# Kernel optimization log

Measured on AMD Instinct MI355X. Metric: run time of the kernel, lower is better.

## Reference

```python
import jax, jax.numpy as jnp
import numpy as np

DIM_QK = 1024


def setup_inputs() -> dict:
    key = jax.random.key(0)
    ks = jax.random.split(key, 5)
    B, S, D = 4, 2048, 1024
    return {
        "x": jax.random.normal(ks[0], (B, S, D), dtype=jnp.float32),
        "Wq": jax.random.normal(ks[1], (DIM_QK, D), dtype=jnp.float32) * (D ** -0.5),
        "Wk": jax.random.normal(ks[2], (DIM_QK, D), dtype=jnp.float32) * (D ** -0.5),
        "Wv": jax.random.normal(ks[3], (D, D), dtype=jnp.float32) * (D ** -0.5),
        "Wo": jax.random.normal(ks[4], (D, D), dtype=jnp.float32) * (D ** -0.5),
    }


def reference(x, Wq, Wk, Wv, Wo):
    # torch Linear: y = x @ W.T (no bias)
    q = jnp.einsum('bsd,kd->bsk', x, Wq)
    k = jnp.einsum('bsd,kd->bsk', x, Wk)
    v = jnp.einsum('bsd,vd->bsv', x, Wv)
    scale = (DIM_QK // 2) ** (-0.5)
    dist = jnp.einsum('bqk,btk->bqt', q, k) * scale  # [B,S,S]
    weight = jax.lax.stop_gradient(dist)             # pre-softmax scores (detached)
    attn = jax.nn.softmax(dist, axis=-1)
    ctx = jnp.einsum('bqt,btv->bqv', attn, v)
    out = jnp.einsum('bqv,ev->bqe', ctx, Wo)
    return (out, weight)
```

## Files before the change

### kernel.cpp

```cpp
#include <hip/hip_runtime.h>
#include <stdint.h>

typedef __attribute__((ext_vector_type(8))) short bf16x8;
typedef __attribute__((ext_vector_type(4))) float f32x4;

__device__ __forceinline__ unsigned short f32_to_bf16(float f) {
  union { float f; unsigned int u; } v; v.f = f;
  unsigned int u = v.u;
  u += 0x7fffu + ((u >> 16) & 1u);
  return (unsigned short)(u >> 16);
}

__device__ __forceinline__ void gload_lds16(const unsigned short* g, unsigned short* lds) {
  __builtin_amdgcn_global_load_lds(
      (const __attribute__((address_space(1))) unsigned int*)g,
      (__attribute__((address_space(3))) unsigned int*)lds,
      16, 0, 0);
}

template<int MODE>
__global__ __launch_bounds__(256, 2)
void gemm_bt(const unsigned short* __restrict__ A,
             const unsigned short* __restrict__ Bm,
             void* __restrict__ Cv,
             int M, int N, int K,
             long sA_, long sB_, long sC_,
             float scale)
{
  __shared__ unsigned short sA[128 * 32];
  __shared__ unsigned short sB[128 * 32];

  const int bz = blockIdx.z;
  const unsigned short* Ab = A + (long)bz * sA_;
  const unsigned short* Bb = Bm + (long)bz * sB_;

  const int m0 = blockIdx.x * 128;
  const int n0 = blockIdx.y * 128;

  const int t = threadIdx.x;
  const int lane = t & 63;
  const int w = t >> 6;
  const int wr = (w >> 1) * 64;
  const int wc = (w & 1) * 64;

  f32x4 acc[4][4];
#pragma unroll
  for (int i = 0; i < 4; ++i)
#pragma unroll
    for (int j = 0; j < 4; ++j)
      acc[i][j] = (f32x4){0.f, 0.f, 0.f, 0.f};

  const int r0 = t >> 2;
  const int kc = (t & 3) * 8;
  const unsigned short* Ap0 = Ab + (long)(m0 + r0) * K + kc;
  const unsigned short* Ap1 = Ab + (long)(m0 + r0 + 64) * K + kc;
  const unsigned short* Bp0 = Bb + (long)(n0 + r0) * K + kc;
  const unsigned short* Bp1 = Bb + (long)(n0 + r0 + 64) * K + kc;

  const int lrow = lane & 15;
  const int q8 = (lane >> 4) * 8;

  for (int k0 = 0; k0 < K; k0 += 32) {
    __syncthreads();
    gload_lds16(Ap0 + k0, &sA[t * 8]);
    gload_lds16(Ap1 + k0, &sA[t * 8 + 2048]);
    gload_lds16(Bp0 + k0, &sB[t * 8]);
    gload_lds16(Bp1 + k0, &sB[t * 8 + 2048]);
    __syncthreads();

    bf16x8 af[4], bfr[4];
#pragma unroll
    for (int i = 0; i < 4; ++i) {
      af[i]  = *(const bf16x8*)&sA[(wr + i * 16 + lrow) * 32 + q8];
      bfr[i] = *(const bf16x8*)&sB[(wc + i * 16 + lrow) * 32 + q8];
    }
#pragma unroll
    for (int mi = 0; mi < 4; ++mi)
#pragma unroll
      for (int ni = 0; ni < 4; ++ni)
        acc[mi][ni] = __builtin_amdgcn_mfma_f32_16x16x32_bf16(af[mi], bfr[ni], acc[mi][ni], 0, 0, 0);
  }

  const int cl = lane & 15;
  const int rq = (lane >> 4) * 4;

  if (MODE == 2) {
    float* Cb = (float*)Cv + (long)bz * sC_;
#pragma unroll
    for (int mi = 0; mi < 4; ++mi) {
      const int rowb = m0 + wr + mi * 16 + rq;
#pragma unroll
      for (int ni = 0; ni < 4; ++ni) {
        const int col = n0 + wc + ni * 16 + cl;
#pragma unroll
        for (int r = 0; r < 4; ++r)
          Cb[(long)(rowb + r) * N + col] = acc[mi][ni][r] * scale;
      }
    }
  } else {
    unsigned short* Cb = (unsigned short*)Cv + (long)bz * sC_;
#pragma unroll
    for (int mi = 0; mi < 4; ++mi) {
      const int rowb = m0 + wr + mi * 16 + rq;
#pragma unroll
      for (int ni = 0; ni < 4; ++ni) {
        const int col = n0 + wc + ni * 16 + cl;
#pragma unroll
        for (int r = 0; r < 4; ++r)
          Cb[(long)(rowb + r) * N + col] = f32_to_bf16(acc[mi][ni][r]);
      }
    }
  }
}

__global__ __launch_bounds__(256)
void softmax_rows(const float* __restrict__ dist, unsigned short* __restrict__ attn) {
  const long row = blockIdx.x;
  const float4* in = (const float4*)(dist + row * 2048);
  const int t = threadIdx.x;
  float4 v0 = in[t];
  float4 v1 = in[t + 256];

  float m = fmaxf(fmaxf(fmaxf(v0.x, v0.y), fmaxf(v0.z, v0.w)),
                  fmaxf(fmaxf(v1.x, v1.y), fmaxf(v1.z, v1.w)));
#pragma unroll
  for (int off = 32; off > 0; off >>= 1)
    m = fmaxf(m, __shfl_xor(m, off, 64));

  __shared__ float redm[4];
  __shared__ float reds[4];
  if ((t & 63) == 0) redm[t >> 6] = m;
  __syncthreads();
  m = fmaxf(fmaxf(redm[0], redm[1]), fmaxf(redm[2], redm[3]));

  float e[8];
  e[0] = __expf(v0.x - m); e[1] = __expf(v0.y - m);
  e[2] = __expf(v0.z - m); e[3] = __expf(v0.w - m);
  e[4] = __expf(v1.x - m); e[5] = __expf(v1.y - m);
  e[6] = __expf(v1.z - m); e[7] = __expf(v1.w - m);

  float s = ((e[0] + e[1]) + (e[2] + e[3])) + ((e[4] + e[5]) + (e[6] + e[7]));
#pragma unroll
  for (int off = 32; off > 0; off >>= 1)
    s += __shfl_xor(s, off, 64);
  if ((t & 63) == 0) reds[t >> 6] = s;
  __syncthreads();
  s = (reds[0] + reds[1]) + (reds[2] + reds[3]);

  const float inv = 1.0f / s;
  ushort4 o0, o1;
  o0.x = f32_to_bf16(e[0] * inv); o0.y = f32_to_bf16(e[1] * inv);
  o0.z = f32_to_bf16(e[2] * inv); o0.w = f32_to_bf16(e[3] * inv);
  o1.x = f32_to_bf16(e[4] * inv); o1.y = f32_to_bf16(e[5] * inv);
  o1.z = f32_to_bf16(e[6] * inv); o1.w = f32_to_bf16(e[7] * inv);
  *(ushort4*)(attn + row * 2048 + t * 4) = o0;
  *(ushort4*)(attn + row * 2048 + 1024 + t * 4) = o1;
}

__global__ __launch_bounds__(256)
void cast_f32_bf16(const float* __restrict__ in, unsigned short* __restrict__ out, int n) {
  const int i = (blockIdx.x * 256 + threadIdx.x) * 4;
  if (i < n) {
    float4 v = *(const float4*)(in + i);
    ushort4 o;
    o.x = f32_to_bf16(v.x); o.y = f32_to_bf16(v.y);
    o.z = f32_to_bf16(v.z); o.w = f32_to_bf16(v.w);
    *(ushort4*)(out + i) = o;
  }
}

extern "C" void kernel_launch(void* const* d_in, const int* in_sizes, int n_in,
                              void* d_out, int out_size, void* d_ws, size_t ws_size,
                              hipStream_t stream) {
  const float* x  = (const float*)d_in[0];
  const float* Wq = (const float*)d_in[1];
  const float* Wk = (const float*)d_in[2];
  const float* Wv = (const float*)d_in[3];
  const float* Wo = (const float*)d_in[4];

  const long Bn = 4, S = 2048, D = 1024;
  const long MS = Bn * S;

  float* out_p  = (float*)d_out;
  float* weight = out_p + MS * D;

  unsigned short* Wqb = (unsigned short*)d_ws;
  unsigned short* Wkb = Wqb + D * D;
  unsigned short* Wvb = Wkb + D * D;
  unsigned short* Wob = Wvb + D * D;
  unsigned short* xb  = Wob + D * D;
  unsigned short* qb  = xb + MS * D;
  unsigned short* kb  = qb + MS * D;
  unsigned short* vtb = kb + MS * D;
  unsigned short* attn = qb;
  unsigned short* ctx  = xb;

  cast_f32_bf16<<<1024, 256, 0, stream>>>(Wq, Wqb, (int)(D * D));
  cast_f32_bf16<<<1024, 256, 0, stream>>>(Wk, Wkb, (int)(D * D));
  cast_f32_bf16<<<1024, 256, 0, stream>>>(Wv, Wvb, (int)(D * D));
  cast_f32_bf16<<<1024, 256, 0, stream>>>(Wo, Wob, (int)(D * D));
  cast_f32_bf16<<<8192, 256, 0, stream>>>(x, xb, (int)(MS * D));

  gemm_bt<0><<<dim3(64, 8, 1), 256, 0, stream>>>(xb, Wqb, qb, 8192, 1024, 1024, 0, 0, 0, 1.f);
  gemm_bt<0><<<dim3(64, 8, 1), 256, 0, stream>>>(xb, Wkb, kb, 8192, 1024, 1024, 0, 0, 0, 1.f);
  gemm_bt<0><<<dim3(8, 16, 4), 256, 0, stream>>>(Wvb, xb, vtb, 1024, 2048, 1024,
                                                 0, S * D, D * S, 1.f);
  gemm_bt<2><<<dim3(16, 16, 4), 256, 0, stream>>>(qb, kb, weight, 2048, 2048, 1024,
                                                  S * D, S * D, S * S, 0.04419417382415922f);
  softmax_rows<<<(int)(Bn * S), 256, 0, stream>>>(weight, attn);
  gemm_bt<0><<<dim3(16, 8, 4), 256, 0, stream>>>(attn, vtb, ctx, 2048, 1024, 2048,
                                                 S * S, D * S, S * D, 1.f);
  gemm_bt<2><<<dim3(64, 8, 1), 256, 0, stream>>>(ctx, Wob, out_p, 8192, 1024, 1024,
                                                 0, 0, 0, 1.f);
}
```

Measured before the change: 354.4 us.

## Fuse Q/K projections, merge cast kernels, and double GEMM K-step per barrier

Concatenates Wq and Wk into one weight so Q and K come out of a single GEMM into an interleaved [MS,2048] buffer, and adds explicit leading dimensions so later GEMMs read Q and K from it. All five f32->bf16 casts merge into one launch. The GEMM main loop now loads 64 K-elements per barrier pair into 32 KB of LDS, halving synchronisations per K step. Raising LDS use to 32 KB per block may affect occupancy, and the loads are still not overlapped with compute.

```diff
diff --git a/kernel.cpp b/kernel.cpp
--- a/kernel.cpp
+++ b/kernel.cpp
@@ -23,12 +23,12 @@
 void gemm_bt(const unsigned short* __restrict__ A,
              const unsigned short* __restrict__ Bm,
              void* __restrict__ Cv,
-             int M, int N, int K,
+             int M, int N, int K, int lda, int ldb, int ldc,
              long sA_, long sB_, long sC_,
              float scale)
 {
-  __shared__ unsigned short sA[128 * 32];
-  __shared__ unsigned short sB[128 * 32];
+  __shared__ unsigned short sA[2 * 128 * 32];
+  __shared__ unsigned short sB[2 * 128 * 32];
 
   const int bz = blockIdx.z;
   const unsigned short* Ab = A + (long)bz * sA_;
@@ -52,33 +52,40 @@
 
   const int r0 = t >> 2;
   const int kc = (t & 3) * 8;
-  const unsigned short* Ap0 = Ab + (long)(m0 + r0) * K + kc;
-  const unsigned short* Ap1 = Ab + (long)(m0 + r0 + 64) * K + kc;
-  const unsigned short* Bp0 = Bb + (long)(n0 + r0) * K + kc;
-  const unsigned short* Bp1 = Bb + (long)(n0 + r0 + 64) * K + kc;
+  const unsigned short* Ap0 = Ab + (long)(m0 + r0) * lda + kc;
+  const unsigned short* Ap1 = Ab + (long)(m0 + r0 + 64) * lda + kc;
+  const unsigned short* Bp0 = Bb + (long)(n0 + r0) * ldb + kc;
+  const unsigned short* Bp1 = Bb + (long)(n0 + r0 + 64) * ldb + kc;
 
   const int lrow = lane & 15;
   const int q8 = (lane >> 4) * 8;
 
-  for (int k0 = 0; k0 < K; k0 += 32) {
+  for (int k0 = 0; k0 < K; k0 += 64) {
     __syncthreads();
-    gload_lds16(Ap0 + k0, &sA[t * 8]);
-    gload_lds16(Ap1 + k0, &sA[t * 8 + 2048]);
-    gload_lds16(Bp0 + k0, &sB[t * 8]);
-    gload_lds16(Bp1 + k0, &sB[t * 8 + 2048]);
+    gload_lds16(Ap0 + k0,      &sA[t * 8]);
+    gload_lds16(Ap1 + k0,      &sA[t * 8 + 2048]);
+    gload_lds16(Ap0 + k0 + 32, &sA[4096 + t * 8]);
+    gload_lds16(Ap1 + k0 + 32, &sA[4096 + t * 8 + 2048]);
+    gload_lds16(Bp0 + k0,      &sB[t * 8]);
+    gload_lds16(Bp1 + k0,      &sB[t * 8 + 2048]);
+    gload_lds16(Bp0 + k0 + 32, &sB[4096 + t * 8]);
+    gload_lds16(Bp1 + k0 + 32, &sB[4096 + t * 8 + 2048]);
     __syncthreads();
 
-    bf16x8 af[4], bfr[4];
-#pragma unroll
-    for (int i = 0; i < 4; ++i) {
-      af[i]  = *(const bf16x8*)&sA[(wr + i * 16 + lrow) * 32 + q8];
-      bfr[i] = *(const bf16x8*)&sB[(wc + i * 16 + lrow) * 32 + q8];
+#pragma unroll
+    for (int s = 0; s < 2; ++s) {
+      bf16x8 af[4], bfr[4];
+#pragma unroll
+      for (int i = 0; i < 4; ++i) {
+        af[i]  = *(const bf16x8*)&sA[s * 4096 + (wr + i * 16 + lrow) * 32 + q8];
+        bfr[i] = *(const bf16x8*)&sB[s * 4096 + (wc + i * 16 + lrow) * 32 + q8];
+      }
+#pragma unroll
+      for (int mi = 0; mi < 4; ++mi)
+#pragma unroll
+        for (int ni = 0; ni < 4; ++ni)
+          acc[mi][ni] = __builtin_amdgcn_mfma_f32_16x16x32_bf16(af[mi], bfr[ni], acc[mi][ni], 0, 0, 0);
     }
-#pragma unroll
-    for (int mi = 0; mi < 4; ++mi)
-#pragma unroll
-      for (int ni = 0; ni < 4; ++ni)
-        acc[mi][ni] = __builtin_amdgcn_mfma_f32_16x16x32_bf16(af[mi], bfr[ni], acc[mi][ni], 0, 0, 0);
   }
 
   const int cl = lane & 15;
@@ -94,7 +101,7 @@
         const int col = n0 + wc + ni * 16 + cl;
 #pragma unroll
         for (int r = 0; r < 4; ++r)
-          Cb[(long)(rowb + r) * N + col] = acc[mi][ni][r] * scale;
+          Cb[(long)(rowb + r) * ldc + col] = acc[mi][ni][r] * scale;
       }
     }
   } else {
@@ -107,7 +114,7 @@
         const int col = n0 + wc + ni * 16 + cl;
 #pragma unroll
         for (int r = 0; r < 4; ++r)
-          Cb[(long)(rowb + r) * N + col] = f32_to_bf16(acc[mi][ni][r]);
+          Cb[(long)(rowb + r) * ldc + col] = f32_to_bf16(acc[mi][ni][r]);
       }
     }
   }
@@ -158,15 +165,25 @@
 }
 
 __global__ __launch_bounds__(256)
-void cast_f32_bf16(const float* __restrict__ in, unsigned short* __restrict__ out, int n) {
-  const int i = (blockIdx.x * 256 + threadIdx.x) * 4;
-  if (i < n) {
-    float4 v = *(const float4*)(in + i);
-    ushort4 o;
-    o.x = f32_to_bf16(v.x); o.y = f32_to_bf16(v.y);
-    o.z = f32_to_bf16(v.z); o.w = f32_to_bf16(v.w);
-    *(ushort4*)(out + i) = o;
+void cast_all(const float* __restrict__ Wq, const float* __restrict__ Wk,
+              const float* __restrict__ Wv, const float* __restrict__ Wo,
+              const float* __restrict__ x, unsigned short* __restrict__ dst) {
+  const long i = ((long)blockIdx.x * 256 + threadIdx.x) * 4;
+  const float* src;
+  long off;
+  if (i < 4194304) {
+    const int which = (int)(i >> 20);
+    src = (which == 0) ? Wq : (which == 1) ? Wk : (which == 2) ? Wv : Wo;
+    off = i & 1048575;
+  } else {
+    src = x;
+    off = i - 4194304;
   }
+  float4 v = *(const float4*)(src + off);
+  ushort4 o;
+  o.x = f32_to_bf16(v.x); o.y = f32_to_bf16(v.y);
+  o.z = f32_to_bf16(v.z); o.w = f32_to_bf16(v.w);
+  *(ushort4*)(dst + i) = o;
 }
 
 extern "C" void kernel_launch(void* const* d_in, const int* in_sizes, int n_in,
@@ -185,31 +202,28 @@
   float* weight = out_p + MS * D;
 
   unsigned short* Wqb = (unsigned short*)d_ws;
-  unsigned short* Wkb = Wqb + D * D;
-  unsigned short* Wvb = Wkb + D * D;
+  unsigned short* Wvb = Wqb + 2 * D * D;
   unsigned short* Wob = Wvb + D * D;
   unsigned short* xb  = Wob + D * D;
-  unsigned short* qb  = xb + MS * D;
-  unsigned short* kb  = qb + MS * D;
-  unsigned short* vtb = kb + MS * D;
-  unsigned short* attn = qb;
+  unsigned short* qk  = xb + MS * D;
+  unsigned short* vtb = qk + MS * 2048;
+  unsigned short* attn = qk;
   unsigned short* ctx  = xb;
 
-  cast_f32_bf16<<<1024, 256, 0, stream>>>(Wq, Wqb, (int)(D * D));
-  cast_f32_bf16<<<1024, 256, 0, stream>>>(Wk, Wkb, (int)(D * D));
-  cast_f32_bf16<<<1024, 256, 0, stream>>>(Wv, Wvb, (int)(D * D));
-  cast_f32_bf16<<<1024, 256, 0, stream>>>(Wo, Wob, (int)(D * D));
-  cast_f32_bf16<<<8192, 256, 0, stream>>>(x, xb, (int)(MS * D));
-
-  gemm_bt<0><<<dim3(64, 8, 1), 256, 0, stream>>>(xb, Wqb, qb, 8192, 1024, 1024, 0, 0, 0, 1.f);
-  gemm_bt<0><<<dim3(64, 8, 1), 256, 0, stream>>>(xb, Wkb, kb, 8192, 1024, 1024, 0, 0, 0, 1.f);
+  cast_all<<<12288, 256, 0, stream>>>(Wq, Wk, Wv, Wo, x, Wqb);
+
+  gemm_bt<0><<<dim3(64, 16, 1), 256, 0, stream>>>(xb, Wqb, qk, 8192, 2048, 1024,
+                                                  1024, 1024, 2048, 0, 0, 0, 1.f);
   gemm_bt<0><<<dim3(8, 16, 4), 256, 0, stream>>>(Wvb, xb, vtb, 1024, 2048, 1024,
-                                                 0, S * D, D * S, 1.f);
-  gemm_bt<2><<<dim3(16, 16, 4), 256, 0, stream>>>(qb, kb, weight, 2048, 2048, 1024,
-                                                  S * D, S * D, S * S, 0.04419417382415922f);
+                                                 1024, 1024, 2048, 0, S * D, D * S, 1.f);
+  gemm_bt<2><<<dim3(16, 16, 4), 256, 0, stream>>>(qk, qk + 1024, weight, 2048, 2048, 1024,
+                                                  2048, 2048, 2048,
+                                                  S * 2048, S * 2048, S * S,
+                                                  0.04419417382415922f);
   softmax_rows<<<(int)(Bn * S), 256, 0, stream>>>(weight, attn);
   gemm_bt<0><<<dim3(16, 8, 4), 256, 0, stream>>>(attn, vtb, ctx, 2048, 1024, 2048,
+                                                 2048, 2048, 1024,
                                                  S * S, D * S, S * D, 1.f);
   gemm_bt<2><<<dim3(64, 8, 1), 256, 0, stream>>>(ctx, Wob, out_p, 8192, 1024, 1024,
-                                                 0, 0, 0, 1.f);
-}
+                                                 1024, 1024, 1024, 0, 0, 0, 1.f);
+}
```

New measurement: 313.8 us. 11.5% less time.
